# Performance work log

Hardware: AMD Instinct MI355X
Metric: run time of the kernel (lower is better)

Reference implementation:

```python
import jax, jax.numpy as jnp
import numpy as np

ALPHA = 0.0005
TAU = 0.2


def setup_inputs() -> dict:
    key = jax.random.key(0)
    k1, k2, k3 = jax.random.split(key, 3)
    x_batch = jax.random.normal(k1, (2048, 4096), dtype=jnp.float32)
    y_batch = jax.random.normal(k2, (2048, 4096), dtype=jnp.float32)
    # conv weight [out_ch, in_ch, kh, kw]; sliced along dim 2 (F = 64)
    conv_w = jax.random.normal(k3, (512, 512, 64, 3), dtype=jnp.float32) * 0.05
    return {"x_batch": x_batch, "y_batch": y_batch, "conv_w": conv_w}


def _diversity_reg(conv_w, tau):
    # slices conv_w[:, :, i, :] flattened -> rows of v: [F, out*in*kw]
    F = conv_w.shape[2]
    v = jnp.transpose(conv_w, (2, 0, 1, 3)).reshape(F, -1)
    norms = jnp.sqrt(jnp.sum(v * v, axis=1))  # [F]
    gram = v @ v.T  # [F, F] -- memory-bound tall-skinny reduction
    sim = gram / (norms[:, None] * norms[None, :])
    eye = jnp.eye(F, dtype=bool)
    # keep iff tau < sim <= 1 and i != j; zeroed entries are detached (constant 0)
    mask = (sim > tau) & (sim <= 1.0) & (~eye)
    return jnp.sum(jnp.where(mask, sim, 0.0))


def reference(x_batch, y_batch, conv_w):
    # loss_function = MSELoss (mean reduction)
    loss_value = jnp.mean((x_batch - y_batch) ** 2)
    reg_value = _diversity_reg(conv_w, TAU)
    return loss_value + ALPHA * reg_value
```

## Files before the change

kernel.cpp:

```cpp
#include <hip/hip_runtime.h>

typedef __attribute__((ext_vector_type(8)))  short   short8;
typedef __attribute__((ext_vector_type(4)))  unsigned uint4v;
typedef __attribute__((ext_vector_type(16))) float   f32x16;

typedef const __attribute__((address_space(1))) unsigned cglb_u32;
typedef __attribute__((address_space(3))) unsigned lds_u32;

constexpr int GRAM_BLOCKS = 256;
constexpr int MSE_BLOCKS  = 256;
constexpr int BLOCK       = 128;
constexpr int SLAB_F      = 192;
constexpr int CHUNK_SLABS = 16;
constexpr int CHUNK_F     = CHUNK_SLABS * SLAB_F;
constexpr int NSLAB       = 512 * 512;
constexpr int NCHUNK      = NSLAB / CHUNK_SLABS;
constexpr int GRAM_WAVES  = GRAM_BLOCKS * (BLOCK / 64);
constexpr int CHUNKS_PER_WAVE = NCHUNK / GRAM_WAVES;
constexpr unsigned MSE_N4 = 2097152u;
constexpr int MSE_THREADS = MSE_BLOCKS * BLOCK;


__device__ __forceinline__ unsigned pk_bf16(float a, float b) {
  unsigned ua = (__builtin_bit_cast(unsigned, a) + 0x8000u) >> 16;
  unsigned ub = (__builtin_bit_cast(unsigned, b) + 0x8000u) & 0xFFFF0000u;
  return ua | ub;
}

__device__ __forceinline__ void stage_chunk(const float* g, float* buf, int lane) {
#pragma unroll
  for (int i = 0; i < 12; ++i) {
    __builtin_amdgcn_global_load_lds(
        (cglb_u32*)(const unsigned*)(g + i * 256 + lane * 4),
        (lds_u32*)(unsigned*)(buf + i * 256),
        16, 0, 0);
  }
}

__global__ __launch_bounds__(BLOCK) void k_main(
    const float* __restrict__ X, const float* __restrict__ Y,
    const float* __restrict__ W, float* __restrict__ ws) {
  __shared__ float lds[2][2][CHUNK_F];
  const int bid = blockIdx.x;
  const int tid = threadIdx.x;

  if (bid >= GRAM_BLOCKS) {
    const int t0 = (bid - GRAM_BLOCKS) * BLOCK + tid;
    const float4* x4 = (const float4*)X;
    const float4* y4 = (const float4*)Y;
    float acc = 0.f;
    for (unsigned i = (unsigned)t0; i < MSE_N4; i += (unsigned)MSE_THREADS) {
      float4 a = x4[i], b = y4[i];
      float d0 = a.x - b.x, d1 = a.y - b.y, d2 = a.z - b.z, d3 = a.w - b.w;
      acc += d0 * d0 + d1 * d1 + d2 * d2 + d3 * d3;
    }
#pragma unroll
    for (int o = 32; o; o >>= 1) acc += __shfl_xor(acc, o, 64);
    if ((tid & 63) == 0) atomicAdd(&ws[0], acc);
    return;
  }

  const int wave = tid >> 6;
  const int lane = tid & 63;
  const int r    = lane & 31;
  const int hi   = lane >> 5;
  const int wg   = bid * 2 + wave;
  const int c0   = wg * CHUNKS_PER_WAVE;

  float* b0 = &lds[wave][0][0];
  float* b1 = &lds[wave][1][0];

  stage_chunk(W + (size_t)c0 * CHUNK_F, b0, lane);

  f32x16 a00{}, a01{}, a11{};

  for (int t = 0; t < CHUNKS_PER_WAVE; ++t) {
    float* cur = (t & 1) ? b1 : b0;
    if (t + 1 < CHUNKS_PER_WAVE) {
      stage_chunk(W + (size_t)(c0 + t + 1) * CHUNK_F, (t & 1) ? b0 : b1, lane);
      asm volatile("s_waitcnt vmcnt(12)" ::: "memory");
    } else {
      asm volatile("s_waitcnt vmcnt(0)" ::: "memory");
    }
    __builtin_amdgcn_sched_barrier(0);

    unsigned fl[3][4], fh[3][4];
#pragma unroll
    for (int bp = 0; bp < 4; ++bp) {
      const float* sA = cur + (hi * 8 + 2 * bp) * SLAB_F + r * 3;
      const float* sB = sA + SLAB_F;
      float a0 = sA[0],  a1 = sA[1],  a2 = sA[2];
      float c0f = sA[96], c1f = sA[97], c2f = sA[98];
      float b0f = sB[0],  b1f = sB[1],  b2f = sB[2];
      float d0f = sB[96], d1f = sB[97], d2f = sB[98];
      fl[0][bp] = pk_bf16(a0, b0f);
      fl[1][bp] = pk_bf16(a1, b1f);
      fl[2][bp] = pk_bf16(a2, b2f);
      fh[0][bp] = pk_bf16(c0f, d0f);
      fh[1][bp] = pk_bf16(c1f, d1f);
      fh[2][bp] = pk_bf16(c2f, d2f);
    }
#pragma unroll
    for (int k = 0; k < 3; ++k) {
      uint4v vl = {fl[k][0], fl[k][1], fl[k][2], fl[k][3]};
      uint4v vh = {fh[k][0], fh[k][1], fh[k][2], fh[k][3]};
      short8 lo = __builtin_bit_cast(short8, vl);
      short8 hv = __builtin_bit_cast(short8, vh);
      a00 = __builtin_amdgcn_mfma_f32_32x32x16_bf16(lo, lo, a00, 0, 0, 0);
      a01 = __builtin_amdgcn_mfma_f32_32x32x16_bf16(lo, hv, a01, 0, 0, 0);
      a11 = __builtin_amdgcn_mfma_f32_32x32x16_bf16(hv, hv, a11, 0, 0, 0);
    }
  }

  __syncthreads();
  float* red = &lds[0][0][0];
  const int base = wave * 3072;
#pragma unroll
  for (int rg = 0; rg < 16; ++rg) {
    red[base +        rg * 64 + lane] = a00[rg];
    red[base + 1024 + rg * 64 + lane] = a01[rg];
    red[base + 2048 + rg * 64 + lane] = a11[rg];
  }
  __syncthreads();
  float* gram = ws + 64;
  for (int e = tid; e < 3072; e += BLOCK)
    atomicAdd(&gram[e], red[e] + red[3072 + e]);
}

__global__ __launch_bounds__(256) void k_fin(const float* __restrict__ ws,
                                             float* __restrict__ out) {
  __shared__ float g[3072];
  __shared__ float n2[64];
  __shared__ float wsum[4];
  const int tid = threadIdx.x;

  for (int e = tid; e < 3072; e += 256) g[e] = ws[64 + e];
  __syncthreads();

  for (int e = tid; e < 3072; e += 256) {
    int tl = e >> 10, rg = (e >> 6) & 15, l = e & 63;
    int il = (rg & 3) + 8 * (rg >> 2) + 4 * (l >> 5);
    int jl = l & 31;
    if (tl != 1 && il == jl) n2[il + (tl == 2 ? 32 : 0)] = g[e];
  }
  __syncthreads();

  float local = 0.f;
  for (int e = tid; e < 3072; e += 256) {
    int tl = e >> 10, rg = (e >> 6) & 15, l = e & 63;
    int il = (rg & 3) + 8 * (rg >> 2) + 4 * (l >> 5);
    int jl = l & 31;
    int i, j; float wgt;
    if (tl == 0)      { i = il;      j = jl;      wgt = 1.f; }
    else if (tl == 1) { i = il;      j = jl + 32; wgt = 2.f; }
    else              { i = il + 32; j = jl + 32; wgt = 1.f; }
    if (i != j) {
      float sim = g[e] / sqrtf(n2[i] * n2[j]);
      if (sim > 0.2f && sim <= 1.0f) local += wgt * sim;
    }
  }
#pragma unroll
  for (int o = 32; o; o >>= 1) local += __shfl_xor(local, o, 64);
  if ((tid & 63) == 0) wsum[tid >> 6] = local;
  __syncthreads();
  if (tid == 0) {
    float reg_sum = wsum[0] + wsum[1] + wsum[2] + wsum[3];
    out[0] = ws[0] * (1.0f / 8388608.0f) + 0.0005f * reg_sum;
  }
}

extern "C" void kernel_launch(void* const* d_in, const int* in_sizes, int n_in,
                              void* d_out, int out_size, void* d_ws, size_t ws_size,
                              hipStream_t stream) {
  const float* X = (const float*)d_in[0];
  const float* Y = (const float*)d_in[1];
  const float* W = (const float*)d_in[2];
  float* ws = (float*)d_ws;

  hipMemsetAsync(d_ws, 0, (64 + 3072) * sizeof(float), stream);
  k_main<<<GRAM_BLOCKS + MSE_BLOCKS, BLOCK, 0, stream>>>(X, Y, W, ws);
  k_fin<<<1, 256, 0, stream>>>(ws, (float*)d_out);
}
```

Measured before the change: 62.91 us.

## Load gram chunks directly into registers and widen blocks to four waves

The LDS staging through global_load_lds with manual waitcnt is replaced by direct global loads of each lane's data into registers, with the next chunk software-prefetched while the current one is processed by MFMA. The block grows to 256 threads (four waves), so each wave handles half as many chunks and the MSE grid gets twice as many threads. The bf16 packing now uses a single perm instruction, and the cross-wave reduction goes through a two-buffer LDS add. The aim is to cut LDS traffic and raise memory parallelism. The costs are higher register pressure and 12-byte loads that may not coalesce well.

```diff
diff --git a/kernel.cpp b/kernel.cpp
--- a/kernel.cpp
+++ b/kernel.cpp
@@ -4,12 +4,9 @@
 typedef __attribute__((ext_vector_type(4)))  unsigned uint4v;
 typedef __attribute__((ext_vector_type(16))) float   f32x16;
 
-typedef const __attribute__((address_space(1))) unsigned cglb_u32;
-typedef __attribute__((address_space(3))) unsigned lds_u32;
-
 constexpr int GRAM_BLOCKS = 256;
 constexpr int MSE_BLOCKS  = 256;
-constexpr int BLOCK       = 128;
+constexpr int BLOCK       = 256;
 constexpr int SLAB_F      = 192;
 constexpr int CHUNK_SLABS = 16;
 constexpr int CHUNK_F     = CHUNK_SLABS * SLAB_F;
@@ -21,26 +18,51 @@
 constexpr int MSE_THREADS = MSE_BLOCKS * BLOCK;
 
 
+struct F3 { float v[3]; };
+struct Chunk { F3 a0[4], a1[4], b0[4], b1[4]; };
+
 __device__ __forceinline__ unsigned pk_bf16(float a, float b) {
-  unsigned ua = (__builtin_bit_cast(unsigned, a) + 0x8000u) >> 16;
-  unsigned ub = (__builtin_bit_cast(unsigned, b) + 0x8000u) & 0xFFFF0000u;
-  return ua | ub;
+  unsigned a2 = __builtin_bit_cast(unsigned, a) + 0x8000u;
+  unsigned b2 = __builtin_bit_cast(unsigned, b) + 0x8000u;
+  return __builtin_amdgcn_perm(b2, a2, 0x07060302u);
 }
 
-__device__ __forceinline__ void stage_chunk(const float* g, float* buf, int lane) {
+__device__ __forceinline__ void load_chunk(const float* __restrict__ s, int laneoff,
+                                           Chunk& c) {
 #pragma unroll
-  for (int i = 0; i < 12; ++i) {
-    __builtin_amdgcn_global_load_lds(
-        (cglb_u32*)(const unsigned*)(g + i * 256 + lane * 4),
-        (lds_u32*)(unsigned*)(buf + i * 256),
-        16, 0, 0);
+  for (int bp = 0; bp < 4; ++bp) {
+    const float* p = s + laneoff + bp * 384;
+    c.a0[bp] = *(const F3*)(p);
+    c.a1[bp] = *(const F3*)(p + 96);
+    c.b0[bp] = *(const F3*)(p + 192);
+    c.b1[bp] = *(const F3*)(p + 288);
   }
 }
 
-__global__ __launch_bounds__(BLOCK) void k_main(
+__device__ __forceinline__ void mac_chunk(const Chunk& c, f32x16& a00, f32x16& a01,
+                                          f32x16& a11) {
+#pragma unroll
+  for (int k = 0; k < 3; ++k) {
+    unsigned fl[4], fh[4];
+#pragma unroll
+    for (int bp = 0; bp < 4; ++bp) {
+      fl[bp] = pk_bf16(c.a0[bp].v[k], c.b0[bp].v[k]);
+      fh[bp] = pk_bf16(c.a1[bp].v[k], c.b1[bp].v[k]);
+    }
+    uint4v vl = {fl[0], fl[1], fl[2], fl[3]};
+    uint4v vh = {fh[0], fh[1], fh[2], fh[3]};
+    short8 lo = __builtin_bit_cast(short8, vl);
+    short8 hv = __builtin_bit_cast(short8, vh);
+    a00 = __builtin_amdgcn_mfma_f32_32x32x16_bf16(lo, lo, a00, 0, 0, 0);
+    a01 = __builtin_amdgcn_mfma_f32_32x32x16_bf16(lo, hv, a01, 0, 0, 0);
+    a11 = __builtin_amdgcn_mfma_f32_32x32x16_bf16(hv, hv, a11, 0, 0, 0);
+  }
+}
+
+__global__ __launch_bounds__(BLOCK, 2) void k_main(
     const float* __restrict__ X, const float* __restrict__ Y,
     const float* __restrict__ W, float* __restrict__ ws) {
-  __shared__ float lds[2][2][CHUNK_F];
+  __shared__ float red[2][3072];
   const int bid = blockIdx.x;
   const int tid = threadIdx.x;
 
@@ -64,67 +86,43 @@
   const int lane = tid & 63;
   const int r    = lane & 31;
   const int hi   = lane >> 5;
-  const int wg   = bid * 2 + wave;
-  const int c0   = wg * CHUNKS_PER_WAVE;
-
-  float* b0 = &lds[wave][0][0];
-  float* b1 = &lds[wave][1][0];
-
-  stage_chunk(W + (size_t)c0 * CHUNK_F, b0, lane);
+  const int wg   = bid * 4 + wave;
+  const int laneoff = hi * 1536 + 3 * r;
+  const float* base = W + (size_t)(wg * CHUNKS_PER_WAVE) * CHUNK_F;
 
   f32x16 a00{}, a01{}, a11{};
+  Chunk ca, cb;
+  load_chunk(base, laneoff, ca);
+#pragma unroll
+  for (int t = 0; t < CHUNKS_PER_WAVE; t += 2) {
+    load_chunk(base + (t + 1) * CHUNK_F, laneoff, cb);
+    mac_chunk(ca, a00, a01, a11);
+    if (t + 2 < CHUNKS_PER_WAVE) load_chunk(base + (t + 2) * CHUNK_F, laneoff, ca);
+    mac_chunk(cb, a00, a01, a11);
+  }
 
-  for (int t = 0; t < CHUNKS_PER_WAVE; ++t) {
-    float* cur = (t & 1) ? b1 : b0;
-    if (t + 1 < CHUNKS_PER_WAVE) {
-      stage_chunk(W + (size_t)(c0 + t + 1) * CHUNK_F, (t & 1) ? b0 : b1, lane);
-      asm volatile("s_waitcnt vmcnt(12)" ::: "memory");
-    } else {
-      asm volatile("s_waitcnt vmcnt(0)" ::: "memory");
-    }
-    __builtin_amdgcn_sched_barrier(0);
-
-    unsigned fl[3][4], fh[3][4];
+  if (wave < 2) {
 #pragma unroll
-    for (int bp = 0; bp < 4; ++bp) {
-      const float* sA = cur + (hi * 8 + 2 * bp) * SLAB_F + r * 3;
-      const float* sB = sA + SLAB_F;
-      float a0 = sA[0],  a1 = sA[1],  a2 = sA[2];
-      float c0f = sA[96], c1f = sA[97], c2f = sA[98];
-      float b0f = sB[0],  b1f = sB[1],  b2f = sB[2];
-      float d0f = sB[96], d1f = sB[97], d2f = sB[98];
-      fl[0][bp] = pk_bf16(a0, b0f);
-      fl[1][bp] = pk_bf16(a1, b1f);
-      fl[2][bp] = pk_bf16(a2, b2f);
-      fh[0][bp] = pk_bf16(c0f, d0f);
-      fh[1][bp] = pk_bf16(c1f, d1f);
-      fh[2][bp] = pk_bf16(c2f, d2f);
-    }
-#pragma unroll
-    for (int k = 0; k < 3; ++k) {
-      uint4v vl = {fl[k][0], fl[k][1], fl[k][2], fl[k][3]};
-      uint4v vh = {fh[k][0], fh[k][1], fh[k][2], fh[k][3]};
-      short8 lo = __builtin_bit_cast(short8, vl);
-      short8 hv = __builtin_bit_cast(short8, vh);
-      a00 = __builtin_amdgcn_mfma_f32_32x32x16_bf16(lo, lo, a00, 0, 0, 0);
-      a01 = __builtin_amdgcn_mfma_f32_32x32x16_bf16(lo, hv, a01, 0, 0, 0);
-      a11 = __builtin_amdgcn_mfma_f32_32x32x16_bf16(hv, hv, a11, 0, 0, 0);
+    for (int rg = 0; rg < 16; ++rg) {
+      red[wave][       rg * 64 + lane] = a00[rg];
+      red[wave][1024 + rg * 64 + lane] = a01[rg];
+      red[wave][2048 + rg * 64 + lane] = a11[rg];
     }
   }
-
   __syncthreads();
-  float* red = &lds[0][0][0];
-  const int base = wave * 3072;
+  if (wave >= 2) {
+    float* dst = red[wave - 2];
 #pragma unroll
-  for (int rg = 0; rg < 16; ++rg) {
-    red[base +        rg * 64 + lane] = a00[rg];
-    red[base + 1024 + rg * 64 + lane] = a01[rg];
-    red[base + 2048 + rg * 64 + lane] = a11[rg];
+    for (int rg = 0; rg < 16; ++rg) {
+      dst[       rg * 64 + lane] += a00[rg];
+      dst[1024 + rg * 64 + lane] += a01[rg];
+      dst[2048 + rg * 64 + lane] += a11[rg];
+    }
   }
   __syncthreads();
   float* gram = ws + 64;
   for (int e = tid; e < 3072; e += BLOCK)
-    atomicAdd(&gram[e], red[e] + red[3072 + e]);
+    atomicAdd(&gram[e], red[0][e] + red[1][e]);
 }
 
 __global__ __launch_bounds__(256) void k_fin(const float* __restrict__ ws,
```

Result: slower. 64.34 us (+2.3%).
